# Kernel optimization log

Measured on AMD Instinct MI355X. Metric: run time of the kernel, lower is better.

Reference implementation:

```python
import jax, jax.numpy as jnp
import numpy as np

EPS_COS = 1e-8   # torch F.cosine_similarity eps
EPS_L1 = 1e-12   # torch F.normalize eps


def setup_inputs() -> dict:
    key = jax.random.key(0)
    k1, k2, k3, k4 = jax.random.split(key, 4)
    B, D, C = 32768, 768, 200
    features = jax.random.normal(k1, (B, D), dtype=jnp.float32)
    centers = jax.random.normal(k2, (C, D), dtype=jnp.float32)
    labels = jax.random.randint(k3, (B,), 0, C)
    labelled_or_not = jax.random.randint(k4, (B,), 0, 2).astype(jnp.bool_)
    return {"features": features, "centers": centers, "labels": labels,
            "labelled_or_not": labelled_or_not}


def reference(features, centers, labels, labelled_or_not):
    # cosine similarity: x.y / (max(|x|,eps) * max(|y|,eps))
    fn = features / jnp.maximum(jnp.linalg.norm(features, axis=1, keepdims=True), EPS_COS)
    cn = centers / jnp.maximum(jnp.linalg.norm(centers, axis=1, keepdims=True), EPS_COS)
    cos = jnp.einsum('bd,cd->bc', fn, cn)  # [B, C]

    # per-sample sign logic: label column -> +|cos|, all others -> -|cos|
    a = jnp.abs(cos)
    is_label = jax.nn.one_hot(labels, cos.shape[1], dtype=jnp.bool_)  # [B, C]
    signed = jnp.where(is_label, a, -a)

    # L1 normalize per row (||row||_1 == sum of |cos| regardless of signs)
    l1 = jnp.sum(a, axis=1, keepdims=True)
    normed = signed / jnp.maximum(l1, EPS_L1)

    # only labelled rows contribute (row-wise normalize is independent per row,
    # so masking after is equivalent to boolean-indexing before)
    contrib = jnp.where(labelled_or_not[:, None], normed, 0.0)
    return -jnp.sum(contrib)
```

## Files before the change

kernel.cpp:

```cpp
#include <hip/hip_runtime.h>
#include <hip/hip_bf16.h>

#define NROWS 32768
#define DIMS  768
#define NC    200
#define CPAD  256
#define KSTEP 32
#define NSTEP (DIMS / KSTEP)
#define ROWSB 64

typedef __attribute__((ext_vector_type(8))) short short8;
typedef __attribute__((ext_vector_type(4))) float f32x4;

#define WAITV2 asm volatile("s_waitcnt vmcnt(2)" ::: "memory")
#define WAITL0 asm volatile("s_waitcnt lgkmcnt(0)" ::: "memory")
#define BAR    __builtin_amdgcn_s_barrier()

__device__ __forceinline__ unsigned pk_bf16(float lo, float hi) {
  union { __hip_bfloat162 h; unsigned u; } c;
  c.h = __float22bfloat162_rn(make_float2(lo, hi));
  return c.u;
}

__global__ __launch_bounds__(256) void prep_centers_k(const float* __restrict__ centers,
                                                      short* __restrict__ cnb2,
                                                      float* __restrict__ out) {
  const int c = blockIdx.x;
  const int tid = threadIdx.x;
  if (c == 0 && tid == 0) out[0] = 0.f;
  if (c >= NC) {
    for (int d = tid; d < DIMS; d += 256)
      cnb2[(d >> 5) * (CPAD * KSTEP) + c * KSTEP + (d & 31)] = 0;
    return;
  }
  float ssq = 0.f;
  for (int d = tid; d < DIMS; d += 256) {
    float v = centers[c * DIMS + d];
    ssq += v * v;
  }
#pragma unroll
  for (int off = 32; off > 0; off >>= 1) ssq += __shfl_down(ssq, off);
  __shared__ float red[4];
  const int wid = tid >> 6, lane = tid & 63;
  if (lane == 0) red[wid] = ssq;
  __syncthreads();
  const float tot = red[0] + red[1] + red[2] + red[3];
  const float inv = 1.f / fmaxf(sqrtf(tot), 1e-8f);
  for (int d = tid; d < DIMS; d += 256) {
    const float v = centers[c * DIMS + d] * inv;
    union { __hip_bfloat16 h; short s; } cv;
    cv.h = __float2bfloat16(v);
    cnb2[(d >> 5) * (CPAD * KSTEP) + c * KSTEP + (d & 31)] = cv.s;
  }
}

__global__ __launch_bounds__(512, 4) void cos_loss_k(
    const float* __restrict__ feats,
    const short* __restrict__ cnb2,
    const int* __restrict__ labels,
    const int* __restrict__ labelled,
    float* __restrict__ out) {
  const int tid = threadIdx.x;
  const int wid = tid >> 6;
  const int lane = tid & 63;
  const int rowBase = blockIdx.x * ROWSB;

  __shared__ short As[2][ROWSB][32];
  __shared__ float l1part[4][ROWSB];
  __shared__ float alpart[4][ROWSB];

  if (wid < 4) {
    const int m = lane & 15;
    const int kg = lane >> 4;
    const int rdq = (kg ^ ((m >> 1) & 3)) * 8;
    const short* bp = cnb2 + (size_t)(wid * 64 + m) * KSTEP + kg * 8;

    f32x4 acc[4][4];
#pragma unroll
    for (int mi = 0; mi < 4; ++mi)
#pragma unroll
      for (int ni = 0; ni < 4; ++ni) acc[mi][ni] = (f32x4){0.f, 0.f, 0.f, 0.f};

    short8 B[4];

#define BLOAD(ni, s) \
    B[ni] = *(const short8*)(bp + (size_t)(s) * (CPAD * KSTEP) + (ni) * (16 * KSTEP))

    BLOAD(0, 0); BLOAD(1, 0); BLOAD(2, 0); BLOAD(3, 0);
    BAR;

#define PHASEC(p, ab) do {                                               \
    const int sn_ = ((p) + 1 < NSTEP) ? (p) + 1 : NSTEP - 1;             \
    short8 af[4];                                                        \
    _Pragma("unroll")                                                    \
    for (int mi = 0; mi < 4; ++mi)                                       \
      af[mi] = *(const short8*)(&As[(ab)][mi * 16 + m][rdq]);            \
    __builtin_amdgcn_s_setprio(1);                                       \
    _Pragma("unroll")                                                    \
    for (int ni = 0; ni < 4; ++ni) {                                     \
      _Pragma("unroll")                                                  \
      for (int mi = 0; mi < 4; ++mi)                                     \
        acc[mi][ni] = __builtin_amdgcn_mfma_f32_16x16x32_bf16(           \
            af[mi], B[ni], acc[mi][ni], 0, 0, 0);                        \
      BLOAD(ni, sn_);                                                    \
    }                                                                    \
    __builtin_amdgcn_s_setprio(0);                                       \
    BAR;                                                                 \
  } while (0)

    for (int p = 0; p < NSTEP; p += 2) {
      PHASEC(p, 0);
      PHASEC(p + 1, 1);
    }
#undef BLOAD
#undef PHASEC

#pragma unroll
    for (int mi = 0; mi < 4; ++mi) {
      float l1r[4] = {0.f, 0.f, 0.f, 0.f};
      float alr[4] = {0.f, 0.f, 0.f, 0.f};
      int labr[4];
#pragma unroll
      for (int r = 0; r < 4; ++r)
        labr[r] = labels[rowBase + mi * 16 + kg * 4 + r];
#pragma unroll
      for (int ni = 0; ni < 4; ++ni) {
        const int col = wid * 64 + ni * 16 + m;
#pragma unroll
        for (int r = 0; r < 4; ++r) {
          const float a = fabsf(acc[mi][ni][r]);
          l1r[r] += a;
          if (col == labr[r]) alr[r] += a;
        }
      }
#pragma unroll
      for (int r = 0; r < 4; ++r) {
#pragma unroll
        for (int off = 1; off < 16; off <<= 1) {
          l1r[r] += __shfl_xor(l1r[r], off);
          alr[r] += __shfl_xor(alr[r], off);
        }
      }
      if (m == 0) {
#pragma unroll
        for (int r = 0; r < 4; ++r) {
          l1part[wid][mi * 16 + kg * 4 + r] = l1r[r];
          alpart[wid][mi * 16 + kg * 4 + r] = alr[r];
        }
      }
    }
  } else {
    const int pt = (wid - 4) * 64 + lane;
    const int arow = pt >> 2;
    const int aq   = pt & 3;
    const int aswz = (arow >> 1) & 3;
    const float* asrc = feats + (size_t)(rowBase + arow) * DIMS + aq * 8;
    short* adst0 = &As[0][arow][(aq ^ aswz) * 8];
    short* adst1 = &As[1][arow][(aq ^ aswz) * 8];

    float4 S0lo, S0hi, S1lo, S1hi;

#define LOADA(P, s) do {                                                 \
    const float* ap_ = asrc + (s) * KSTEP;                               \
    P##lo = *(const float4*)(ap_);                                       \
    P##hi = *(const float4*)(ap_ + 4);                                   \
  } while (0)

#define WRITEA(P, dst) do {                                              \
    union { short8 s8; unsigned u[4]; } p_;                              \
    p_.u[0] = pk_bf16(P##lo.x, P##lo.y);                                 \
    p_.u[1] = pk_bf16(P##lo.z, P##lo.w);                                 \
    p_.u[2] = pk_bf16(P##hi.x, P##hi.y);                                 \
    p_.u[3] = pk_bf16(P##hi.z, P##hi.w);                                 \
    *(short8*)(dst) = p_.s8;                                             \
  } while (0)

#define CLMP(x) (((x) < NSTEP) ? (x) : NSTEP - 1)

    LOADA(S0, 0);
    LOADA(S1, 1);
    WAITV2;
    WRITEA(S0, adst0);
    WAITL0;
    BAR;

    for (int p = 0; p < NSTEP; p += 2) {
      LOADA(S0, CLMP(p + 2));
      WAITV2;
      WRITEA(S1, adst1);
      WAITL0;
      BAR;
      LOADA(S1, CLMP(p + 3));
      WAITV2;
      WRITEA(S0, adst0);
      WAITL0;
      BAR;
    }
#undef LOADA
#undef WRITEA
#undef CLMP
  }

  __syncthreads();

  if (tid < ROWSB) {
    const float L = l1part[0][tid] + l1part[1][tid] + l1part[2][tid] + l1part[3][tid];
    const float A = alpart[0][tid] + alpart[1][tid] + alpart[2][tid] + alpart[3][tid];
    float c = labelled[rowBase + tid] ? (L - 2.f * A) / fmaxf(L, 1e-12f) : 0.f;
#pragma unroll
    for (int off = 1; off < 64; off <<= 1) c += __shfl_xor(c, off);
    if (tid == 0) atomicAdd(out, c);
  }
}

extern "C" void kernel_launch(void* const* d_in, const int* in_sizes, int n_in,
                              void* d_out, int out_size, void* d_ws, size_t ws_size,
                              hipStream_t stream) {
  const float* feats = (const float*)d_in[0];
  const float* centers = (const float*)d_in[1];
  const int* labels = (const int*)d_in[2];
  const int* labelled = (const int*)d_in[3];
  float* out = (float*)d_out;
  short* cnb2 = (short*)d_ws;

  prep_centers_k<<<CPAD, 256, 0, stream>>>(centers, cnb2, out);
  cos_loss_k<<<NROWS / ROWSB, 512, 0, stream>>>(feats, cnb2, labels, labelled, out);
}
```

Baseline: 35.50 us.

## Deepen feature staging pipeline to four LDS buffers with longer prefetch distance

Expands the shared-memory A staging from two to four bf16 buffers. Producer waves now write a tile two steps ahead of the compute waves and issue global loads four steps ahead, giving each feature load more time to arrive before it must be converted. LDS usage per block doubles for the A tiles, which could limit occupancy, and the buffer rotation must stay in step with the consumer's barrier sequence.

```diff
diff --git a/kernel.cpp b/kernel.cpp
--- a/kernel.cpp
+++ b/kernel.cpp
@@ -65,7 +65,7 @@
   const int lane = tid & 63;
   const int rowBase = blockIdx.x * ROWSB;
 
-  __shared__ short As[2][ROWSB][32];
+  __shared__ short As[4][ROWSB][32];
   __shared__ float l1part[4][ROWSB];
   __shared__ float alpart[4][ROWSB];
 
@@ -89,12 +89,12 @@
     BLOAD(0, 0); BLOAD(1, 0); BLOAD(2, 0); BLOAD(3, 0);
     BAR;
 
-#define PHASEC(p, ab) do {                                               \
+#define PHASEC(p, rb) do {                                               \
     const int sn_ = ((p) + 1 < NSTEP) ? (p) + 1 : NSTEP - 1;             \
     short8 af[4];                                                        \
     _Pragma("unroll")                                                    \
     for (int mi = 0; mi < 4; ++mi)                                       \
-      af[mi] = *(const short8*)(&As[(ab)][mi * 16 + m][rdq]);            \
+      af[mi] = *(const short8*)(&As[(rb)][mi * 16 + m][rdq]);            \
     __builtin_amdgcn_s_setprio(1);                                       \
     _Pragma("unroll")                                                    \
     for (int ni = 0; ni < 4; ++ni) {                                     \
@@ -108,9 +108,11 @@
     BAR;                                                                 \
   } while (0)
 
-    for (int p = 0; p < NSTEP; p += 2) {
-      PHASEC(p, 0);
+    for (int p = 0; p < NSTEP; p += 4) {
+      PHASEC(p,     0);
       PHASEC(p + 1, 1);
+      PHASEC(p + 2, 2);
+      PHASEC(p + 3, 3);
     }
 #undef BLOAD
 #undef PHASEC
@@ -155,8 +157,7 @@
     const int aq   = pt & 3;
     const int aswz = (arow >> 1) & 3;
     const float* asrc = feats + (size_t)(rowBase + arow) * DIMS + aq * 8;
-    short* adst0 = &As[0][arow][(aq ^ aswz) * 8];
-    short* adst1 = &As[1][arow][(aq ^ aswz) * 8];
+    const int aoff = (aq ^ aswz) * 8;
 
     float4 S0lo, S0hi, S1lo, S1hi;
 
@@ -166,13 +167,13 @@
     P##hi = *(const float4*)(ap_ + 4);                                   \
   } while (0)
 
-#define WRITEA(P, dst) do {                                              \
+#define WRITEA(P, rb) do {                                               \
     union { short8 s8; unsigned u[4]; } p_;                              \
     p_.u[0] = pk_bf16(P##lo.x, P##lo.y);                                 \
     p_.u[1] = pk_bf16(P##lo.z, P##lo.w);                                 \
     p_.u[2] = pk_bf16(P##hi.x, P##hi.y);                                 \
     p_.u[3] = pk_bf16(P##hi.z, P##hi.w);                                 \
-    *(short8*)(dst) = p_.s8;                                             \
+    *(short8*)(&As[(rb)][arow][aoff]) = p_.s8;                           \
   } while (0)
 
 #define CLMP(x) (((x) < NSTEP) ? (x) : NSTEP - 1)
@@ -180,24 +181,31 @@
     LOADA(S0, 0);
     LOADA(S1, 1);
     WAITV2;
-    WRITEA(S0, adst0);
+    WRITEA(S0, 0);
+    LOADA(S0, 2);
+    WAITV2;
+    WRITEA(S1, 1);
+    LOADA(S1, 3);
     WAITL0;
     BAR;
 
-    for (int p = 0; p < NSTEP; p += 2) {
-      LOADA(S0, CLMP(p + 2));
-      WAITV2;
-      WRITEA(S1, adst1);
-      WAITL0;
-      BAR;
-      LOADA(S1, CLMP(p + 3));
-      WAITV2;
-      WRITEA(S0, adst0);
-      WAITL0;
-      BAR;
+#define PHASEP(p, SL, rb) do {                                           \
+    WAITV2;             \
+    WRITEA(SL, rb);                                                      \
+    LOADA(SL, CLMP((p) + 4));                                            \
+    WAITL0;                                                              \
+    BAR;                                                                 \
+  } while (0)
+
+    for (int p = 0; p < NSTEP; p += 4) {
+      PHASEP(p,     S0, 2);
+      PHASEP(p + 1, S1, 3);
+      PHASEP(p + 2, S0, 0);
+      PHASEP(p + 3, S1, 1);
     }
 #undef LOADA
 #undef WRITEA
+#undef PHASEP
 #undef CLMP
   }
 
```

Result: slower. 37.90 us (+6.8%).
